# Kernel optimization log

Measured on AMD Instinct MI355X. Metric: run time of the kernel, lower is better.

The kernel has to match this reference:

```python
import jax, jax.numpy as jnp
import numpy as np

NH = 8  # num_heads
EPS_LN = 1e-5
BN_DENOM = float(np.sqrt(1.0 + 1e-5))  # eval-mode BN with running_mean=0, running_var=1


def _layernorm(x, g, b):
    m = jnp.mean(x, axis=-1, keepdims=True)
    v = jnp.var(x, axis=-1, keepdims=True)
    return (x - m) * jax.lax.rsqrt(v + EPS_LN) * g + b


def _rope(q, k):
    # q,k: [B, H, T, D]
    t, d = q.shape[2], q.shape[3]
    half = d // 2
    pos = jnp.arange(t, dtype=q.dtype)[:, None]
    idx = jnp.arange(half, dtype=q.dtype)[None, :]
    inv_freq = 1.0 / (10000.0 ** (idx / half))
    ang = pos * inv_freq  # [T, half]
    sin = jnp.sin(ang)[None, None]
    cos = jnp.cos(ang)[None, None]

    def rot(x):
        x1, x2 = x[..., :half], x[..., half:]
        return jnp.concatenate([x1 * cos - x2 * sin, x1 * sin + x2 * cos], axis=-1)

    return rot(q), rot(k)


def _sep_conv(y, dw, pw):
    # y: [B, C, T]; dw: [C, 1, K]; pw: [O, C]
    c = y.shape[1]
    k = dw.shape[-1]
    y = jax.lax.conv_general_dilated(
        y, dw, window_strides=(2,), padding=[(k // 2, k // 2)],
        dimension_numbers=('NCH', 'OIH', 'NCH'), feature_group_count=c)
    return jnp.einsum('bct,oc->bot', y, pw)


def _attn(h, Wq, bq, Wk, bk, Wv, bv, Wo, bo):
    b, t, e = h.shape
    hd = e // NH
    scale = hd ** -0.5

    def split(z):
        return jnp.transpose(z.reshape(b, t, NH, hd), (0, 2, 1, 3))

    q = split(h @ Wq.T + bq)
    k = split(h @ Wk.T + bk)
    v = split(h @ Wv.T + bv)
    q, k = _rope(q, k)
    logits = jnp.einsum('bhtd,bhsd->bhts', q, k) * scale
    attn = jax.nn.softmax(logits, axis=-1)
    ctx = jnp.einsum('bhts,bhsd->bhtd', attn, v)
    ctx = jnp.transpose(ctx, (0, 2, 1, 3)).reshape(b, t, e)
    return ctx @ Wo.T + bo


def setup_inputs() -> dict:
    key = jax.random.key(0)
    ks = jax.random.split(key, 40)
    B, T, Cin = 8, 4096, 64
    E, L, MLP = 256, 6, 1024
    s = 0.02
    p = {}
    p['x'] = jax.random.normal(ks[0], (B, T, Cin), jnp.float32)
    p['conv1_dw'] = jax.random.normal(ks[1], (Cin, 1, 7), jnp.float32) * s
    p['conv1_pw'] = jax.random.normal(ks[2], (64, Cin), jnp.float32) * s
    p['bn1_g'] = jnp.ones((64,), jnp.float32)
    p['bn1_b'] = jnp.zeros((64,), jnp.float32)
    p['conv2_dw'] = jax.random.normal(ks[3], (64, 1, 7), jnp.float32) * s
    p['conv2_pw'] = jax.random.normal(ks[4], (128, 64), jnp.float32) * s
    p['bn2_g'] = jnp.ones((128,), jnp.float32)
    p['bn2_b'] = jnp.zeros((128,), jnp.float32)
    p['proj_w'] = jax.random.normal(ks[5], (E, 128), jnp.float32) * s
    p['proj_b'] = jnp.zeros((E,), jnp.float32)
    p['cls_tok'] = jax.random.normal(ks[6], (1, 1, E), jnp.float32) * s
    p['Wq'] = jax.random.normal(ks[7], (L, E, E), jnp.float32) * s
    p['bq'] = jnp.zeros((L, E), jnp.float32)
    p['Wk'] = jax.random.normal(ks[8], (L, E, E), jnp.float32) * s
    p['bk'] = jnp.zeros((L, E), jnp.float32)
    p['Wv'] = jax.random.normal(ks[9], (L, E, E), jnp.float32) * s
    p['bv'] = jnp.zeros((L, E), jnp.float32)
    p['Wo'] = jax.random.normal(ks[10], (L, E, E), jnp.float32) * s
    p['bo'] = jnp.zeros((L, E), jnp.float32)
    p['ln1_g'] = jnp.ones((L, E), jnp.float32)
    p['ln1_b'] = jnp.zeros((L, E), jnp.float32)
    p['mlp_w1'] = jax.random.normal(ks[11], (L, MLP, E), jnp.float32) * s
    p['mlp_b1'] = jnp.zeros((L, MLP), jnp.float32)
    p['mlp_w2'] = jax.random.normal(ks[12], (L, E, MLP), jnp.float32) * s
    p['mlp_b2'] = jnp.zeros((L, E), jnp.float32)
    p['ln2_g'] = jnp.ones((L, E), jnp.float32)
    p['ln2_b'] = jnp.zeros((L, E), jnp.float32)
    p['lat_w'] = jax.random.normal(ks[13], (E, E), jnp.float32) * s
    p['lat_b'] = jnp.zeros((E,), jnp.float32)
    p['latn_g'] = jnp.ones((E,), jnp.float32)
    p['latn_b'] = jnp.zeros((E,), jnp.float32)
    p['ts_w'] = jax.random.normal(ks[14], (1, E), jnp.float32) * s
    p['ts_b'] = jnp.zeros((1,), jnp.float32)
    return p


def reference(x, conv1_dw, conv1_pw, bn1_g, bn1_b, conv2_dw, conv2_pw, bn2_g, bn2_b,
              proj_w, proj_b, cls_tok, Wq, bq, Wk, bk, Wv, bv, Wo, bo,
              ln1_g, ln1_b, mlp_w1, mlp_b1, mlp_w2, mlp_b2, ln2_g, ln2_b,
              lat_w, lat_b, latn_g, latn_b, ts_w, ts_b):
    B = x.shape[0]
    y = jnp.transpose(x, (0, 2, 1))  # [B, C, T]
    y = _sep_conv(y, conv1_dw, conv1_pw)
    y = (y / BN_DENOM) * bn1_g[None, :, None] + bn1_b[None, :, None]
    y = jax.nn.gelu(y, approximate=False)
    y = _sep_conv(y, conv2_dw, conv2_pw)
    y = (y / BN_DENOM) * bn2_g[None, :, None] + bn2_b[None, :, None]
    y = jax.nn.gelu(y, approximate=False)
    y = jnp.transpose(y, (0, 2, 1))  # [B, T', 128]
    h = y @ proj_w.T + proj_b  # [B, T', E]
    h = jnp.concatenate([jnp.broadcast_to(cls_tok, (B, 1, h.shape[-1])), h], axis=1)
    L = Wq.shape[0]
    for i in range(L):
        a = _attn(h, Wq[i], bq[i], Wk[i], bk[i], Wv[i], bv[i], Wo[i], bo[i])
        h = _layernorm(h + a, ln1_g[i], ln1_b[i])
        m = jax.nn.gelu(h @ mlp_w1[i].T + mlp_b1[i], approximate=False) @ mlp_w2[i].T + mlp_b2[i]
        h = _layernorm(h + m, ln2_g[i], ln2_b[i])
    h = _layernorm(h @ lat_w.T + lat_b, latn_g, latn_b)
    logits = h[:, 1:] @ ts_w.T + ts_b  # per-time-step logits (CLS excluded)
    return logits
```

## Files before the change

### kernel.cpp

```cpp
#include <hip/hip_runtime.h>
#include <hip/hip_bf16.h>
#include <math.h>

typedef __hip_bfloat16 bf16;
typedef __attribute__((ext_vector_type(8))) short bf16x8_t;
typedef __attribute__((ext_vector_type(4))) short bf16x4_t;
typedef __attribute__((ext_vector_type(4))) float f32x4_t;

#define BN_RDENOM 0.9999950000374997f
#define EPS_LN 1e-5f
#define ATTN_SCALE 0.17677669529663687f
#define S_LEN 1025
#define S_PAD 1088
#define E_DIM 256
#define NHEAD 8
#define HDIM 32
#define MROWS (8 * S_LEN)

__device__ __forceinline__ float bf(const bf16 v) { return __bfloat162float(v); }
__device__ __forceinline__ bf16 tobf(float v) { return __float2bfloat16(v); }
__device__ __forceinline__ short bfbits(float v) {
    bf16 t = __float2bfloat16(v); short s; __builtin_memcpy(&s, &t, 2); return s;
}
__device__ __forceinline__ float gelu_exact(float x) {
    return 0.5f * x * (1.0f + erff(x * 0.70710678118654752f));
}

#define DPP_ROR(x, N) __int_as_float(__builtin_amdgcn_update_dpp(0, __float_as_int(x), 0x120 + (N), 0xF, 0xF, false))
__device__ __forceinline__ float row_allsum(float x) {
    x = x + DPP_ROR(x, 1);
    x = x + DPP_ROR(x, 2);
    x = x + DPP_ROR(x, 4);
    x = x + DPP_ROR(x, 8);
    return x;
}

__global__ __launch_bounds__(256) void cvt_w(const float* __restrict__ src,
    bf16* __restrict__ dst, int n)
{
    int i = (blockIdx.x * 256 + threadIdx.x) * 4;
    if (i >= n) return;
    f32x4_t v = *(const f32x4_t*)(src + i);
    bf16x4_t o;
    #pragma unroll
    for (int j = 0; j < 4; ++j) o[j] = bfbits(v[j]);
    *(bf16x4_t*)((short*)dst + i) = o;
}

__global__ __launch_bounds__(256) void cvt_layer(const float* __restrict__ wq,
    const float* __restrict__ wk, const float* __restrict__ wv, const float* __restrict__ wo,
    const float* __restrict__ w1, const float* __restrict__ w2, bf16* __restrict__ dst)
{
    int i = (blockIdx.x * 256 + threadIdx.x) * 4;
    const float* s; int off;
    if (i < 262144) {
        s = (i < 65536) ? wq : (i < 131072) ? wk : (i < 196608) ? wv : wo;
        off = i & 65535;
    } else if (i < 524288) { s = w1; off = i - 262144; }
    else                   { s = w2; off = i - 524288; }
    f32x4_t v = *(const f32x4_t*)(s + off);
    bf16x4_t o;
    #pragma unroll
    for (int j = 0; j < 4; ++j) o[j] = bfbits(v[j]);
    *(bf16x4_t*)((short*)dst + i) = o;
}

__global__ __launch_bounds__(256) void conv_sep1(const float* __restrict__ x,
    const float* __restrict__ dw, const float* __restrict__ pw,
    const float* __restrict__ g, const float* __restrict__ bb,
    bf16* __restrict__ out)
{
    __shared__ float xs[70][64];
    __shared__ float dy[32][64];
    __shared__ float pws[64][65];
    __shared__ float dws[64][7];
    int blk = blockIdx.x;
    int tile = blk & 63, b = blk >> 6;
    int t0 = tile * 32;
    int tid = threadIdx.x;
    int tbase = t0 * 2 - 3;
    for (int i = tid; i < 70 * 64; i += 256) {
        int r = i >> 6, c = i & 63;
        int t = tbase + r;
        xs[r][c] = (t >= 0 && t < 4096) ? x[((size_t)b * 4096 + t) * 64 + c] : 0.f;
    }
    for (int i = tid; i < 64 * 7; i += 256) dws[i / 7][i % 7] = dw[i];
    for (int i = tid; i < 64 * 64; i += 256) pws[i >> 6][i & 63] = pw[i];
    __syncthreads();
    for (int i = tid; i < 32 * 64; i += 256) {
        int tl = i >> 6, c = i & 63;
        float s = 0.f;
        #pragma unroll
        for (int j = 0; j < 7; ++j) s += xs[2 * tl + j][c] * dws[c][j];
        dy[tl][c] = s;
    }
    __syncthreads();
    for (int i = tid; i < 32 * 64; i += 256) {
        int tl = i >> 6, o = i & 63;
        float s = 0.f;
        #pragma unroll 8
        for (int c = 0; c < 64; ++c) s += dy[tl][c] * pws[o][c];
        s = s * BN_RDENOM * g[o] + bb[o];
        out[((size_t)(b * 2048 + t0 + tl)) * 64 + o] = tobf(gelu_exact(s));
    }
}

__global__ __launch_bounds__(256) void conv_sep2(const bf16* __restrict__ x,
    const float* __restrict__ dw, const float* __restrict__ pw,
    const float* __restrict__ g, const float* __restrict__ bb,
    bf16* __restrict__ out)
{
    __shared__ float xs[70][64];
    __shared__ float dy[32][64];
    __shared__ float pws[128][65];
    __shared__ float dws[64][7];
    int blk = blockIdx.x;
    int tile = blk & 31, b = blk >> 5;
    int t0 = tile * 32;
    int tid = threadIdx.x;
    int tbase = t0 * 2 - 3;
    for (int i = tid; i < 70 * 64; i += 256) {
        int r = i >> 6, c = i & 63;
        int t = tbase + r;
        xs[r][c] = (t >= 0 && t < 2048) ? bf(x[((size_t)b * 2048 + t) * 64 + c]) : 0.f;
    }
    for (int i = tid; i < 64 * 7; i += 256) dws[i / 7][i % 7] = dw[i];
    for (int i = tid; i < 128 * 64; i += 256) pws[i >> 6][i & 63] = pw[i];
    __syncthreads();
    for (int i = tid; i < 32 * 64; i += 256) {
        int tl = i >> 6, c = i & 63;
        float s = 0.f;
        #pragma unroll
        for (int j = 0; j < 7; ++j) s += xs[2 * tl + j][c] * dws[c][j];
        dy[tl][c] = s;
    }
    __syncthreads();
    for (int i = tid; i < 32 * 128; i += 256) {
        int tl = i >> 7, o = i & 127;
        float s = 0.f;
        #pragma unroll 8
        for (int c = 0; c < 64; ++c) s += dy[tl][c] * pws[o][c];
        s = s * BN_RDENOM * g[o] + bb[o];
        out[((size_t)(b * 1024 + t0 + tl)) * 128 + o] = tobf(gelu_exact(s));
    }
}

template <int ACT>
__global__ __launch_bounds__(256) void gemm_bf(const bf16* __restrict__ A,
    const bf16* __restrict__ W, const float* __restrict__ bias,
    bf16* __restrict__ C, int M, int N, int K)
{
    __shared__ short As[64 * 72];
    __shared__ short Bs[64 * 72];
    int tid = threadIdx.x;
    int wave = tid >> 6, lane = tid & 63, quad = lane >> 4, l16 = lane & 15;
    int wm = wave & 1, wn = wave >> 1;
    int m0 = blockIdx.x * 64, n0 = blockIdx.y * 64;

    f32x4_t zero4 = {0.f, 0.f, 0.f, 0.f};
    f32x4_t acc[2][2];
    acc[0][0] = zero4; acc[0][1] = zero4; acc[1][0] = zero4; acc[1][1] = zero4;

    int srow = tid >> 2, skc = (tid & 3) * 16;
    for (int k0 = 0; k0 < K; k0 += 64) {
        {
            int m = m0 + srow;
            bf16x8_t a0 = {}, a1 = {};
            if (m < M) {
                a0 = *(const bf16x8_t*)(A + (size_t)m * K + k0 + skc);
                a1 = *(const bf16x8_t*)(A + (size_t)m * K + k0 + skc + 8);
            }
            *(bf16x8_t*)(&As[srow * 72 + skc])     = a0;
            *(bf16x8_t*)(&As[srow * 72 + skc + 8]) = a1;
        }
        {
            const bf16* wp = W + (size_t)(n0 + srow) * K + k0 + skc;
            *(bf16x8_t*)(&Bs[srow * 72 + skc])     = *(const bf16x8_t*)(wp);
            *(bf16x8_t*)(&Bs[srow * 72 + skc + 8]) = *(const bf16x8_t*)(wp + 8);
        }
        __syncthreads();
        #pragma unroll
        for (int ks = 0; ks < 2; ++ks) {
            bf16x8_t a[2], b[2];
            #pragma unroll
            for (int mi = 0; mi < 2; ++mi)
                a[mi] = *(bf16x8_t*)(&As[(wm * 32 + mi * 16 + l16) * 72 + ks * 32 + quad * 8]);
            #pragma unroll
            for (int ni = 0; ni < 2; ++ni)
                b[ni] = *(bf16x8_t*)(&Bs[(wn * 32 + ni * 16 + l16) * 72 + ks * 32 + quad * 8]);
            #pragma unroll
            for (int mi = 0; mi < 2; ++mi)
                #pragma unroll
                for (int ni = 0; ni < 2; ++ni)
                    acc[mi][ni] = __builtin_amdgcn_mfma_f32_16x16x32_bf16(a[mi], b[ni], acc[mi][ni], 0, 0, 0);
        }
        __syncthreads();
    }
    #pragma unroll
    for (int mi = 0; mi < 2; ++mi) {
        #pragma unroll
        for (int ni = 0; ni < 2; ++ni) {
            int col = n0 + wn * 32 + ni * 16 + l16;
            float bv = bias[col];
            #pragma unroll
            for (int r = 0; r < 4; ++r) {
                int row = m0 + wm * 32 + mi * 16 + quad * 4 + r;
                if (row < M) {
                    float v = acc[mi][ni][r] + bv;
                    if (ACT == 1) v = gelu_exact(v);
                    C[(size_t)row * N + col] = tobf(v);
                }
            }
        }
    }
}

template <int ACT>
__global__ __launch_bounds__(256) void gemm_bf128(const bf16* __restrict__ A,
    const bf16* __restrict__ W, const float* __restrict__ bias,
    bf16* __restrict__ C, int M, int N, int K)
{
    __shared__ short As[128 * 72];
    __shared__ short Bs[64 * 72];
    int tid = threadIdx.x;
    int wave = tid >> 6, lane = tid & 63, quad = lane >> 4, l16 = lane & 15;
    int wm = wave & 1, wn = wave >> 1;
    int m0 = blockIdx.x * 128, n0 = blockIdx.y * 64;

    f32x4_t zero4 = {0.f, 0.f, 0.f, 0.f};
    f32x4_t acc[4][2];
    #pragma unroll
    for (int i = 0; i < 4; ++i) { acc[i][0] = zero4; acc[i][1] = zero4; }

    int srow = tid >> 2, skc = (tid & 3) * 16;
    for (int k0 = 0; k0 < K; k0 += 64) {
        #pragma unroll
        for (int p = 0; p < 2; ++p) {
            int row = srow + p * 64;
            int m = m0 + row;
            bf16x8_t a0 = {}, a1 = {};
            if (m < M) {
                a0 = *(const bf16x8_t*)(A + (size_t)m * K + k0 + skc);
                a1 = *(const bf16x8_t*)(A + (size_t)m * K + k0 + skc + 8);
            }
            *(bf16x8_t*)(&As[row * 72 + skc])     = a0;
            *(bf16x8_t*)(&As[row * 72 + skc + 8]) = a1;
        }
        {
            const bf16* wp = W + (size_t)(n0 + srow) * K + k0 + skc;
            *(bf16x8_t*)(&Bs[srow * 72 + skc])     = *(const bf16x8_t*)(wp);
            *(bf16x8_t*)(&Bs[srow * 72 + skc + 8]) = *(const bf16x8_t*)(wp + 8);
        }
        __syncthreads();
        #pragma unroll
        for (int ks = 0; ks < 2; ++ks) {
            bf16x8_t a[4], b[2];
            #pragma unroll
            for (int mi = 0; mi < 4; ++mi)
                a[mi] = *(bf16x8_t*)(&As[(wm * 64 + mi * 16 + l16) * 72 + ks * 32 + quad * 8]);
            #pragma unroll
            for (int ni = 0; ni < 2; ++ni)
                b[ni] = *(bf16x8_t*)(&Bs[(wn * 32 + ni * 16 + l16) * 72 + ks * 32 + quad * 8]);
            #pragma unroll
            for (int mi = 0; mi < 4; ++mi)
                #pragma unroll
                for (int ni = 0; ni < 2; ++ni)
                    acc[mi][ni] = __builtin_amdgcn_mfma_f32_16x16x32_bf16(a[mi], b[ni], acc[mi][ni], 0, 0, 0);
        }
        __syncthreads();
    }
    #pragma unroll
    for (int mi = 0; mi < 4; ++mi) {
        #pragma unroll
        for (int ni = 0; ni < 2; ++ni) {
            int col = n0 + wn * 32 + ni * 16 + l16;
            float bv = bias[col];
            #pragma unroll
            for (int r = 0; r < 4; ++r) {
                int row = m0 + wm * 64 + mi * 16 + quad * 4 + r;
                if (row < M) {
                    float v = acc[mi][ni][r] + bv;
                    if (ACT == 1) v = gelu_exact(v);
                    C[(size_t)row * N + col] = tobf(v);
                }
            }
        }
    }
}

__global__ __launch_bounds__(256) void gemm_qkv(const bf16* __restrict__ A,
    const bf16* __restrict__ Wqkv, const float* __restrict__ bq,
    const float* __restrict__ bk, const float* __restrict__ bv,
    bf16* __restrict__ qo, bf16* __restrict__ ko, bf16* __restrict__ vo, int M)
{
    const int K = 256, N = 256;
    __shared__ short As[64 * 72];
    __shared__ short Bs[64 * 72];
    int part = blockIdx.y >> 2;
    int n0 = (blockIdx.y & 3) * 64;
    const bf16* W     = Wqkv + (size_t)part * 65536;
    const float* bias = (part == 0) ? bq : (part == 1) ? bk : bv;
    bf16* C           = (part == 0) ? qo : (part == 1) ? ko : vo;
    bool dorope = (part < 2);
    float oscale = (part == 0) ? ATTN_SCALE : 1.0f;

    int tid = threadIdx.x;
    int wave = tid >> 6, lane = tid & 63, quad = lane >> 4, l16 = lane & 15;
    int wm = wave & 1, wn = wave >> 1;
    int m0 = blockIdx.x * 64;

    f32x4_t zero4 = {0.f, 0.f, 0.f, 0.f};
    f32x4_t acc[2][2];
    acc[0][0] = zero4; acc[0][1] = zero4; acc[1][0] = zero4; acc[1][1] = zero4;

    int srow = tid >> 2, skc = (tid & 3) * 16;
    for (int k0 = 0; k0 < K; k0 += 64) {
        {
            int m = m0 + srow;
            bf16x8_t a0 = {}, a1 = {};
            if (m < M) {
                a0 = *(const bf16x8_t*)(A + (size_t)m * K + k0 + skc);
                a1 = *(const bf16x8_t*)(A + (size_t)m * K + k0 + skc + 8);
            }
            *(bf16x8_t*)(&As[srow * 72 + skc])     = a0;
            *(bf16x8_t*)(&As[srow * 72 + skc + 8]) = a1;
        }
        {
            const bf16* wp = W + (size_t)(n0 + srow) * K + k0 + skc;
            *(bf16x8_t*)(&Bs[srow * 72 + skc])     = *(const bf16x8_t*)(wp);
            *(bf16x8_t*)(&Bs[srow * 72 + skc + 8]) = *(const bf16x8_t*)(wp + 8);
        }
        __syncthreads();
        #pragma unroll
        for (int ks = 0; ks < 2; ++ks) {
            bf16x8_t a[2], b[2];
            #pragma unroll
            for (int mi = 0; mi < 2; ++mi)
                a[mi] = *(bf16x8_t*)(&As[(wm * 32 + mi * 16 + l16) * 72 + ks * 32 + quad * 8]);
            #pragma unroll
            for (int ni = 0; ni < 2; ++ni)
                b[ni] = *(bf16x8_t*)(&Bs[(wn * 32 + ni * 16 + l16) * 72 + ks * 32 + quad * 8]);
            #pragma unroll
            for (int mi = 0; mi < 2; ++mi)
                #pragma unroll
                for (int ni = 0; ni < 2; ++ni)
                    acc[mi][ni] = __builtin_amdgcn_mfma_f32_16x16x32_bf16(a[mi], b[ni], acc[mi][ni], 0, 0, 0);
        }
        __syncthreads();
    }
    int col0 = n0 + wn * 32 + l16;
    float b1v = bias[col0], b2v = bias[col0 + 16];
    float invf = powf(10000.f, -(float)l16 * (1.f / 16.f));
    #pragma unroll
    for (int mi = 0; mi < 2; ++mi) {
        #pragma unroll
        for (int r = 0; r < 4; ++r) {
            int row = m0 + wm * 32 + mi * 16 + quad * 4 + r;
            if (row >= M) continue;
            int bb = row / S_LEN, t = row - bb * S_LEN;
            float x1 = acc[mi][0][r] + b1v;
            float x2 = acc[mi][1][r] + b2v;
            if (dorope) {
                float ang = (float)t * invf;
                float sn, cs;
                __sincosf(ang, &sn, &cs);
                float y1 = (x1 * cs - x2 * sn) * oscale;
                float y2 = (x1 * sn + x2 * cs) * oscale;
                x1 = y1; x2 = y2;
            }
            size_t obase = ((size_t)bb * S_PAD + t) * N;
            C[obase + col0]      = tobf(x1);
            C[obase + col0 + 16] = tobf(x2);
        }
    }
}

__global__ __launch_bounds__(256) void assemble_h(const bf16* __restrict__ tmp,
    const float* __restrict__ cls, bf16* __restrict__ h)
{
    int row = blockIdx.x;
    int tid = threadIdx.x;
    int b = row / S_LEN, t = row % S_LEN;
    bf16 v = (t == 0) ? tobf(cls[tid]) : tmp[((size_t)(b * 1024 + t - 1)) * E_DIM + tid];
    h[(size_t)row * E_DIM + tid] = v;
}

__global__ __launch_bounds__(256) void attn_mfma(const bf16* __restrict__ Q,
    const bf16* __restrict__ K, const bf16* __restrict__ V, bf16* __restrict__ O)
{
    __shared__ short VTs[2][32 * 72];
    __shared__ short Ps[4][16 * 72];
    const int NQT = 17;
    int blk = blockIdx.x;
    int qt = blk % NQT;
    int bh = blk / NQT;
    int hh = bh & 7, b = bh >> 3;
    int tid = threadIdx.x;
    int wave = tid >> 6, lane = tid & 63, quad = lane >> 4, l16 = lane & 15;
    int q0 = qt * 64 + wave * 16;
    const size_t bSp = (size_t)b * S_PAD;
    const size_t bS  = (size_t)b * S_LEN;
    const size_t hoff = (size_t)hh * HDIM;
    const bf16* Qb = Q + bSp * E_DIM + hoff;
    const bf16* Kb = K + bSp * E_DIM + hoff;
    const bf16* Vb = V + bSp * E_DIM + hoff;

    f32x4_t zero4 = {0.f, 0.f, 0.f, 0.f};
    bf16x8_t qfrag = *(const bf16x8_t*)(Qb + (size_t)(q0 + l16) * E_DIM + quad * 8);
    f32x4_t o0 = zero4, o1 = zero4;
    float lrun[4] = {0.f, 0.f, 0.f, 0.f};

    int vs = tid >> 2, vd = (tid & 3) * 8;
    short* myP = Ps[wave];

    bf16x8_t vpre = *(const bf16x8_t*)(Vb + (size_t)vs * E_DIM + vd);

    for (int c = 0; c < 17; ++c) {
        int s0 = c * 64;
        short* VT = VTs[c & 1];
        #pragma unroll
        for (int j = 0; j < 8; ++j) VT[(vd + j) * 72 + vs] = vpre[j];
        if (c < 16)
            vpre = *(const bf16x8_t*)(Vb + (size_t)(s0 + 64 + vs) * E_DIM + vd);
        f32x4_t sc[4];
        #pragma unroll
        for (int kk = 0; kk < 4; ++kk) {
            bf16x8_t kf = *(const bf16x8_t*)(Kb + (size_t)(s0 + kk * 16 + l16) * E_DIM + quad * 8);
            sc[kk] = __builtin_amdgcn_mfma_f32_16x16x32_bf16(qfrag, kf, zero4, 0, 0, 0);
        }
        #pragma unroll
        for (int r = 0; r < 4; ++r) {
            float ps = 0.f;
            #pragma unroll
            for (int kk = 0; kk < 4; ++kk) {
                int s = s0 + kk * 16 + l16;
                float raw = (s < S_LEN) ? sc[kk][r] : -1e30f;
                float p = __expf(raw);
                ps += p;
                myP[(quad * 4 + r) * 72 + kk * 16 + l16] = bfbits(p);
            }
            lrun[r] += row_allsum(ps);
        }
        __syncthreads();
        #pragma unroll
        for (int half = 0; half < 2; ++half) {
            int off = half * 32 + quad * 8;
            bf16x8_t pf  = *(bf16x8_t*)(&myP[l16 * 72 + off]);
            bf16x8_t vf0 = *(bf16x8_t*)(&VTs[c & 1][l16 * 72 + off]);
            bf16x8_t vf1 = *(bf16x8_t*)(&VTs[c & 1][(16 + l16) * 72 + off]);
            o0 = __builtin_amdgcn_mfma_f32_16x16x32_bf16(pf, vf0, o0, 0, 0, 0);
            o1 = __builtin_amdgcn_mfma_f32_16x16x32_bf16(pf, vf1, o1, 0, 0, 0);
        }
    }
    #pragma unroll
    for (int r = 0; r < 4; ++r) {
        int qrow = q0 + quad * 4 + r;
        if (qrow < S_LEN) {
            float rs = 1.f / lrun[r];
            O[(bS + qrow) * E_DIM + hoff + l16]      = tobf(o0[r] * rs);
            O[(bS + qrow) * E_DIM + hoff + 16 + l16] = tobf(o1[r] * rs);
        }
    }
}

__global__ __launch_bounds__(256) void ln_kernel(const bf16* __restrict__ X,
    const bf16* __restrict__ R, const float* __restrict__ g,
    const float* __restrict__ b, bf16* __restrict__ out)
{
    int row = blockIdx.x * 4 + (threadIdx.x >> 6);
    int lane = threadIdx.x & 63;
    size_t base = (size_t)row * E_DIM + lane * 4;
    bf16x4_t xv = *(const bf16x4_t*)(X + base);
    float v[4];
    #pragma unroll
    for (int i = 0; i < 4; ++i) { bf16 t; short s = xv[i]; __builtin_memcpy(&t, &s, 2); v[i] = bf(t); }
    if (R) {
        bf16x4_t rv = *(const bf16x4_t*)(R + base);
        #pragma unroll
        for (int i = 0; i < 4; ++i) { bf16 t; short s = rv[i]; __builtin_memcpy(&t, &s, 2); v[i] += bf(t); }
    }
    float s = v[0] + v[1] + v[2] + v[3];
    #pragma unroll
    for (int off = 32; off; off >>= 1) s += __shfl_xor(s, off);
    float mean = s * (1.f / 256.f);
    float var = 0.f;
    #pragma unroll
    for (int i = 0; i < 4; ++i) { v[i] -= mean; var += v[i] * v[i]; }
    #pragma unroll
    for (int off = 32; off; off >>= 1) var += __shfl_xor(var, off);
    float rstd = rsqrtf(var * (1.f / 256.f) + EPS_LN);
    int c = lane * 4;
    bf16x4_t ov;
    #pragma unroll
    for (int i = 0; i < 4; ++i) ov[i] = bfbits(v[i] * rstd * g[c + i] + b[c + i]);
    *(bf16x4_t*)(out + base) = ov;
}

__global__ __launch_bounds__(256) void ts_kernel(const bf16* __restrict__ H,
    const float* __restrict__ w, const float* __restrict__ tb,
    float* __restrict__ out)
{
    int wid = (blockIdx.x << 2) + (threadIdx.x >> 6);
    int lane = threadIdx.x & 63;
    int b = wid >> 10, t = wid & 1023;
    const bf16* row = H + ((size_t)(b * S_LEN + t + 1)) * E_DIM;
    float acc = 0.f;
    for (int e = lane; e < E_DIM; e += 64) acc += bf(row[e]) * w[e];
    #pragma unroll
    for (int off = 32; off; off >>= 1) acc += __shfl_down(acc, off, 64);
    if (lane == 0) out[wid] = acc + tb[0];
}

extern "C" void kernel_launch(void* const* d_in, const int* in_sizes, int n_in,
                              void* d_out, int out_size, void* d_ws, size_t ws_size,
                              hipStream_t stream)
{
    (void)in_sizes; (void)n_in; (void)out_size; (void)ws_size;
    const float* X        = (const float*)d_in[0];
    const float* CONV1_DW = (const float*)d_in[1];
    const float* CONV1_PW = (const float*)d_in[2];
    const float* BN1_G    = (const float*)d_in[3];
    const float* BN1_B    = (const float*)d_in[4];
    const float* CONV2_DW = (const float*)d_in[5];
    const float* CONV2_PW = (const float*)d_in[6];
    const float* BN2_G    = (const float*)d_in[7];
    const float* BN2_B    = (const float*)d_in[8];
    const float* PROJ_W   = (const float*)d_in[9];
    const float* PROJ_B   = (const float*)d_in[10];
    const float* CLS      = (const float*)d_in[11];
    const float* WQ       = (const float*)d_in[12];
    const float* BQ       = (const float*)d_in[13];
    const float* WK       = (const float*)d_in[14];
    const float* BK       = (const float*)d_in[15];
    const float* WV       = (const float*)d_in[16];
    const float* BV       = (const float*)d_in[17];
    const float* WO       = (const float*)d_in[18];
    const float* BO       = (const float*)d_in[19];
    const float* LN1G     = (const float*)d_in[20];
    const float* LN1B     = (const float*)d_in[21];
    const float* W1       = (const float*)d_in[22];
    const float* B1       = (const float*)d_in[23];
    const float* W2       = (const float*)d_in[24];
    const float* B2       = (const float*)d_in[25];
    const float* LN2G     = (const float*)d_in[26];
    const float* LN2B     = (const float*)d_in[27];
    const float* LATW     = (const float*)d_in[28];
    const float* LATB     = (const float*)d_in[29];
    const float* LATNG    = (const float*)d_in[30];
    const float* LATNB    = (const float*)d_in[31];
    const float* TSW      = (const float*)d_in[32];
    const float* TSB      = (const float*)d_in[33];

    const size_t SROW  = (size_t)MROWS * E_DIM;
    const size_t SPROW = (size_t)8 * S_PAD * E_DIM;
    bf16* h    = (bf16*)d_ws;
    bf16* bufB = h + SROW;
    bf16* r0   = bufB + SROW;
    bf16* q  = r0;
    bf16* k  = r0 + SPROW;
    bf16* v  = r0 + 2 * SPROW;
    bf16* cx = r0 + 3 * SPROW;
    bf16* wslot = cx + SROW;
    bf16* y1 = r0;
    bf16* y2 = r0 + SROW;
    bf16* mid = r0;

    conv_sep1<<<dim3(512), dim3(256), 0, stream>>>(X, CONV1_DW, CONV1_PW, BN1_G, BN1_B, y1);
    conv_sep2<<<dim3(256), dim3(256), 0, stream>>>(y1, CONV2_DW, CONV2_PW, BN2_G, BN2_B, y2);
    cvt_w<<<dim3(32), dim3(256), 0, stream>>>(PROJ_W, wslot, 32768);
    gemm_bf<0><<<dim3(128, 4), dim3(256), 0, stream>>>(y2, wslot, PROJ_B, bufB, 8192, 256, 128);
    assemble_h<<<dim3(MROWS), dim3(256), 0, stream>>>(bufB, CLS, h);

    for (int l = 0; l < 6; ++l) {
        cvt_layer<<<dim3(768), dim3(256), 0, stream>>>(
            WQ + (size_t)l * 65536, WK + (size_t)l * 65536, WV + (size_t)l * 65536,
            WO + (size_t)l * 65536, W1 + (size_t)l * 262144, W2 + (size_t)l * 262144, wslot);
        gemm_qkv<<<dim3(129, 12), dim3(256), 0, stream>>>(h, wslot,
            BQ + l * 256, BK + l * 256, BV + l * 256, q, k, v, MROWS);
        attn_mfma<<<dim3(64 * 17), dim3(256), 0, stream>>>(q, k, v, cx);
        gemm_bf<0><<<dim3(129, 4), dim3(256), 0, stream>>>(cx, wslot + 196608, BO + l * 256, bufB, MROWS, 256, 256);
        ln_kernel<<<dim3(MROWS / 4), dim3(256), 0, stream>>>(h, bufB, LN1G + l * 256, LN1B + l * 256, h);
        gemm_bf128<1><<<dim3(65, 16), dim3(256), 0, stream>>>(h, wslot + 262144, B1 + l * 1024, mid, MROWS, 1024, 256);
        gemm_bf<0><<<dim3(129, 4), dim3(256), 0, stream>>>(mid, wslot + 524288, B2 + l * 256, bufB, MROWS, 256, 1024);
        ln_kernel<<<dim3(MROWS / 4), dim3(256), 0, stream>>>(h, bufB, LN2G + l * 256, LN2B + l * 256, h);
    }

    cvt_w<<<dim3(64), dim3(256), 0, stream>>>(LATW, wslot, 65536);
    gemm_bf<0><<<dim3(129, 4), dim3(256), 0, stream>>>(h, wslot, LATB, bufB, MROWS, 256, 256);
    ln_kernel<<<dim3(MROWS / 4), dim3(256), 0, stream>>>(bufB, nullptr, LATNG, LATNB, r0);
    ts_kernel<<<dim3(2048), dim3(256), 0, stream>>>(r0, TSW, TSB, (float*)d_out);
}
```

Baseline: 879.4 us.

## Double-buffer GEMM shared tiles with register prefetch and defer attention row-sum reduction

The three GEMM kernels now use two shared-memory buffers per operand and prefetch the next K-chunk from global memory into registers while the MFMAs run on the current chunk. This removes one barrier per iteration and hides global load latency. In attention, the per-lane partial softmax sums are accumulated locally and reduced across lanes only once at the end, not on every chunk. The cost is double the shared memory per block, which may lower occupancy.

```diff
diff --git a/kernel.cpp b/kernel.cpp
--- a/kernel.cpp
+++ b/kernel.cpp
@@ -150,8 +150,8 @@
     const bf16* __restrict__ W, const float* __restrict__ bias,
     bf16* __restrict__ C, int M, int N, int K)
 {
-    __shared__ short As[64 * 72];
-    __shared__ short Bs[64 * 72];
+    __shared__ short As[2][64 * 72];
+    __shared__ short Bs[2][64 * 72];
     int tid = threadIdx.x;
     int wave = tid >> 6, lane = tid & 63, quad = lane >> 4, l16 = lane & 15;
     int wm = wave & 1, wn = wave >> 1;
@@ -162,39 +162,43 @@
     acc[0][0] = zero4; acc[0][1] = zero4; acc[1][0] = zero4; acc[1][1] = zero4;
 
     int srow = tid >> 2, skc = (tid & 3) * 16;
-    for (int k0 = 0; k0 < K; k0 += 64) {
-        {
-            int m = m0 + srow;
-            bf16x8_t a0 = {}, a1 = {};
-            if (m < M) {
-                a0 = *(const bf16x8_t*)(A + (size_t)m * K + k0 + skc);
-                a1 = *(const bf16x8_t*)(A + (size_t)m * K + k0 + skc + 8);
-            }
-            *(bf16x8_t*)(&As[srow * 72 + skc])     = a0;
-            *(bf16x8_t*)(&As[srow * 72 + skc + 8]) = a1;
-        }
-        {
-            const bf16* wp = W + (size_t)(n0 + srow) * K + k0 + skc;
-            *(bf16x8_t*)(&Bs[srow * 72 + skc])     = *(const bf16x8_t*)(wp);
-            *(bf16x8_t*)(&Bs[srow * 72 + skc + 8]) = *(const bf16x8_t*)(wp + 8);
-        }
+    bool aok = (m0 + srow) < M;
+    const bf16* ap = A + (size_t)(m0 + srow) * K + skc;
+    const bf16* wp = W + (size_t)(n0 + srow) * K + skc;
+
+    bf16x8_t a0 = {}, a1 = {}, b0, b1;
+    if (aok) { a0 = *(const bf16x8_t*)(ap); a1 = *(const bf16x8_t*)(ap + 8); }
+    b0 = *(const bf16x8_t*)(wp); b1 = *(const bf16x8_t*)(wp + 8);
+
+    int nch = K >> 6;
+    for (int c = 0; c < nch; ++c) {
+        short* AsB = As[c & 1];
+        short* BsB = Bs[c & 1];
+        *(bf16x8_t*)(&AsB[srow * 72 + skc])     = a0;
+        *(bf16x8_t*)(&AsB[srow * 72 + skc + 8]) = a1;
+        *(bf16x8_t*)(&BsB[srow * 72 + skc])     = b0;
+        *(bf16x8_t*)(&BsB[srow * 72 + skc + 8]) = b1;
         __syncthreads();
+        if (c + 1 < nch) {
+            int k0 = (c + 1) << 6;
+            if (aok) { a0 = *(const bf16x8_t*)(ap + k0); a1 = *(const bf16x8_t*)(ap + k0 + 8); }
+            b0 = *(const bf16x8_t*)(wp + k0); b1 = *(const bf16x8_t*)(wp + k0 + 8);
+        }
         #pragma unroll
         for (int ks = 0; ks < 2; ++ks) {
             bf16x8_t a[2], b[2];
             #pragma unroll
             for (int mi = 0; mi < 2; ++mi)
-                a[mi] = *(bf16x8_t*)(&As[(wm * 32 + mi * 16 + l16) * 72 + ks * 32 + quad * 8]);
+                a[mi] = *(bf16x8_t*)(&AsB[(wm * 32 + mi * 16 + l16) * 72 + ks * 32 + quad * 8]);
             #pragma unroll
             for (int ni = 0; ni < 2; ++ni)
-                b[ni] = *(bf16x8_t*)(&Bs[(wn * 32 + ni * 16 + l16) * 72 + ks * 32 + quad * 8]);
+                b[ni] = *(bf16x8_t*)(&BsB[(wn * 32 + ni * 16 + l16) * 72 + ks * 32 + quad * 8]);
             #pragma unroll
             for (int mi = 0; mi < 2; ++mi)
                 #pragma unroll
                 for (int ni = 0; ni < 2; ++ni)
                     acc[mi][ni] = __builtin_amdgcn_mfma_f32_16x16x32_bf16(a[mi], b[ni], acc[mi][ni], 0, 0, 0);
         }
-        __syncthreads();
     }
     #pragma unroll
     for (int mi = 0; mi < 2; ++mi) {
@@ -220,8 +224,8 @@
     const bf16* __restrict__ W, const float* __restrict__ bias,
     bf16* __restrict__ C, int M, int N, int K)
 {
-    __shared__ short As[128 * 72];
-    __shared__ short Bs[64 * 72];
+    __shared__ short As[2][128 * 72];
+    __shared__ short Bs[2][64 * 72];
     int tid = threadIdx.x;
     int wave = tid >> 6, lane = tid & 63, quad = lane >> 4, l16 = lane & 15;
     int wm = wave & 1, wn = wave >> 1;
@@ -233,41 +237,48 @@
     for (int i = 0; i < 4; ++i) { acc[i][0] = zero4; acc[i][1] = zero4; }
 
     int srow = tid >> 2, skc = (tid & 3) * 16;
-    for (int k0 = 0; k0 < K; k0 += 64) {
-        #pragma unroll
-        for (int p = 0; p < 2; ++p) {
-            int row = srow + p * 64;
-            int m = m0 + row;
-            bf16x8_t a0 = {}, a1 = {};
-            if (m < M) {
-                a0 = *(const bf16x8_t*)(A + (size_t)m * K + k0 + skc);
-                a1 = *(const bf16x8_t*)(A + (size_t)m * K + k0 + skc + 8);
-            }
-            *(bf16x8_t*)(&As[row * 72 + skc])     = a0;
-            *(bf16x8_t*)(&As[row * 72 + skc + 8]) = a1;
-        }
-        {
-            const bf16* wp = W + (size_t)(n0 + srow) * K + k0 + skc;
-            *(bf16x8_t*)(&Bs[srow * 72 + skc])     = *(const bf16x8_t*)(wp);
-            *(bf16x8_t*)(&Bs[srow * 72 + skc + 8]) = *(const bf16x8_t*)(wp + 8);
-        }
+    bool aok0 = (m0 + srow) < M, aok1 = (m0 + 64 + srow) < M;
+    const bf16* ap0 = A + (size_t)(m0 + srow) * K + skc;
+    const bf16* ap1 = A + (size_t)(m0 + 64 + srow) * K + skc;
+    const bf16* wp  = W + (size_t)(n0 + srow) * K + skc;
+
+    bf16x8_t a00 = {}, a01 = {}, a10 = {}, a11 = {}, b0, b1;
+    if (aok0) { a00 = *(const bf16x8_t*)(ap0); a01 = *(const bf16x8_t*)(ap0 + 8); }
+    if (aok1) { a10 = *(const bf16x8_t*)(ap1); a11 = *(const bf16x8_t*)(ap1 + 8); }
+    b0 = *(const bf16x8_t*)(wp); b1 = *(const bf16x8_t*)(wp + 8);
+
+    int nch = K >> 6;
+    for (int c = 0; c < nch; ++c) {
+        short* AsB = As[c & 1];
+        short* BsB = Bs[c & 1];
+        *(bf16x8_t*)(&AsB[srow * 72 + skc])            = a00;
+        *(bf16x8_t*)(&AsB[srow * 72 + skc + 8])        = a01;
+        *(bf16x8_t*)(&AsB[(64 + srow) * 72 + skc])     = a10;
+        *(bf16x8_t*)(&AsB[(64 + srow) * 72 + skc + 8]) = a11;
+        *(bf16x8_t*)(&BsB[srow * 72 + skc])            = b0;
+        *(bf16x8_t*)(&BsB[srow * 72 + skc + 8])        = b1;
         __syncthreads();
+        if (c + 1 < nch) {
+            int k0 = (c + 1) << 6;
+            if (aok0) { a00 = *(const bf16x8_t*)(ap0 + k0); a01 = *(const bf16x8_t*)(ap0 + k0 + 8); }
+            if (aok1) { a10 = *(const bf16x8_t*)(ap1 + k0); a11 = *(const bf16x8_t*)(ap1 + k0 + 8); }
+            b0 = *(const bf16x8_t*)(wp + k0); b1 = *(const bf16x8_t*)(wp + k0 + 8);
+        }
         #pragma unroll
         for (int ks = 0; ks < 2; ++ks) {
             bf16x8_t a[4], b[2];
             #pragma unroll
             for (int mi = 0; mi < 4; ++mi)
-                a[mi] = *(bf16x8_t*)(&As[(wm * 64 + mi * 16 + l16) * 72 + ks * 32 + quad * 8]);
+                a[mi] = *(bf16x8_t*)(&AsB[(wm * 64 + mi * 16 + l16) * 72 + ks * 32 + quad * 8]);
             #pragma unroll
             for (int ni = 0; ni < 2; ++ni)
-                b[ni] = *(bf16x8_t*)(&Bs[(wn * 32 + ni * 16 + l16) * 72 + ks * 32 + quad * 8]);
+                b[ni] = *(bf16x8_t*)(&BsB[(wn * 32 + ni * 16 + l16) * 72 + ks * 32 + quad * 8]);
             #pragma unroll
             for (int mi = 0; mi < 4; ++mi)
                 #pragma unroll
                 for (int ni = 0; ni < 2; ++ni)
                     acc[mi][ni] = __builtin_amdgcn_mfma_f32_16x16x32_bf16(a[mi], b[ni], acc[mi][ni], 0, 0, 0);
         }
-        __syncthreads();
     }
     #pragma unroll
     for (int mi = 0; mi < 4; ++mi) {
@@ -294,8 +305,8 @@
     bf16* __restrict__ qo, bf16* __restrict__ ko, bf16* __restrict__ vo, int M)
 {
     const int K = 256, N = 256;
-    __shared__ short As[64 * 72];
-    __shared__ short Bs[64 * 72];
+    __shared__ short As[2][64 * 72];
+    __shared__ short Bs[2][64 * 72];
     int part = blockIdx.y >> 2;
     int n0 = (blockIdx.y & 3) * 64;
     const bf16* W     = Wqkv + (size_t)part * 65536;
@@ -314,39 +325,42 @@
     acc[0][0] = zero4; acc[0][1] = zero4; acc[1][0] = zero4; acc[1][1] = zero4;
 
     int srow = tid >> 2, skc = (tid & 3) * 16;
-    for (int k0 = 0; k0 < K; k0 += 64) {
-        {
-            int m = m0 + srow;
-            bf16x8_t a0 = {}, a1 = {};
-            if (m < M) {
-                a0 = *(const bf16x8_t*)(A + (size_t)m * K + k0 + skc);
-                a1 = *(const bf16x8_t*)(A + (size_t)m * K + k0 + skc + 8);
-            }
-            *(bf16x8_t*)(&As[srow * 72 + skc])     = a0;
-            *(bf16x8_t*)(&As[srow * 72 + skc + 8]) = a1;
-        }
-        {
-            const bf16* wp = W + (size_t)(n0 + srow) * K + k0 + skc;
-            *(bf16x8_t*)(&Bs[srow * 72 + skc])     = *(const bf16x8_t*)(wp);
-            *(bf16x8_t*)(&Bs[srow * 72 + skc + 8]) = *(const bf16x8_t*)(wp + 8);
-        }
+    bool aok = (m0 + srow) < M;
+    const bf16* ap = A + (size_t)(m0 + srow) * K + skc;
+    const bf16* wp = W + (size_t)(n0 + srow) * K + skc;
+
+    bf16x8_t a0 = {}, a1 = {}, b0, b1;
+    if (aok) { a0 = *(const bf16x8_t*)(ap); a1 = *(const bf16x8_t*)(ap + 8); }
+    b0 = *(const bf16x8_t*)(wp); b1 = *(const bf16x8_t*)(wp + 8);
+
+    for (int c = 0; c < 4; ++c) {
+        short* AsB = As[c & 1];
+        short* BsB = Bs[c & 1];
+        *(bf16x8_t*)(&AsB[srow * 72 + skc])     = a0;
+        *(bf16x8_t*)(&AsB[srow * 72 + skc + 8]) = a1;
+        *(bf16x8_t*)(&BsB[srow * 72 + skc])     = b0;
+        *(bf16x8_t*)(&BsB[srow * 72 + skc + 8]) = b1;
         __syncthreads();
+        if (c < 3) {
+            int k0 = (c + 1) << 6;
+            if (aok) { a0 = *(const bf16x8_t*)(ap + k0); a1 = *(const bf16x8_t*)(ap + k0 + 8); }
+            b0 = *(const bf16x8_t*)(wp + k0); b1 = *(const bf16x8_t*)(wp + k0 + 8);
+        }
         #pragma unroll
         for (int ks = 0; ks < 2; ++ks) {
             bf16x8_t a[2], b[2];
             #pragma unroll
             for (int mi = 0; mi < 2; ++mi)
-                a[mi] = *(bf16x8_t*)(&As[(wm * 32 + mi * 16 + l16) * 72 + ks * 32 + quad * 8]);
+                a[mi] = *(bf16x8_t*)(&AsB[(wm * 32 + mi * 16 + l16) * 72 + ks * 32 + quad * 8]);
             #pragma unroll
             for (int ni = 0; ni < 2; ++ni)
-                b[ni] = *(bf16x8_t*)(&Bs[(wn * 32 + ni * 16 + l16) * 72 + ks * 32 + quad * 8]);
+                b[ni] = *(bf16x8_t*)(&BsB[(wn * 32 + ni * 16 + l16) * 72 + ks * 32 + quad * 8]);
             #pragma unroll
             for (int mi = 0; mi < 2; ++mi)
                 #pragma unroll
                 for (int ni = 0; ni < 2; ++ni)
                     acc[mi][ni] = __builtin_amdgcn_mfma_f32_16x16x32_bf16(a[mi], b[ni], acc[mi][ni], 0, 0, 0);
         }
-        __syncthreads();
     }
     int col0 = n0 + wn * 32 + l16;
     float b1v = bias[col0], b2v = bias[col0 + 16];
@@ -408,7 +422,7 @@
     f32x4_t zero4 = {0.f, 0.f, 0.f, 0.f};
     bf16x8_t qfrag = *(const bf16x8_t*)(Qb + (size_t)(q0 + l16) * E_DIM + quad * 8);
     f32x4_t o0 = zero4, o1 = zero4;
-    float lrun[4] = {0.f, 0.f, 0.f, 0.f};
+    float lsum[4] = {0.f, 0.f, 0.f, 0.f};
 
     int vs = tid >> 2, vd = (tid & 3) * 8;
     short* myP = Ps[wave];
@@ -439,15 +453,15 @@
                 ps += p;
                 myP[(quad * 4 + r) * 72 + kk * 16 + l16] = bfbits(p);
             }
-            lrun[r] += row_allsum(ps);
+            lsum[r] += ps;
         }
         __syncthreads();
         #pragma unroll
         for (int half = 0; half < 2; ++half) {
             int off = half * 32 + quad * 8;
             bf16x8_t pf  = *(bf16x8_t*)(&myP[l16 * 72 + off]);
-            bf16x8_t vf0 = *(bf16x8_t*)(&VTs[c & 1][l16 * 72 + off]);
-            bf16x8_t vf1 = *(bf16x8_t*)(&VTs[c & 1][(16 + l16) * 72 + off]);
+            bf16x8_t vf0 = *(bf16x8_t*)(&VT[l16 * 72 + off]);
+            bf16x8_t vf1 = *(bf16x8_t*)(&VT[(16 + l16) * 72 + off]);
             o0 = __builtin_amdgcn_mfma_f32_16x16x32_bf16(pf, vf0, o0, 0, 0, 0);
             o1 = __builtin_amdgcn_mfma_f32_16x16x32_bf16(pf, vf1, o1, 0, 0, 0);
         }
@@ -456,7 +470,7 @@
     for (int r = 0; r < 4; ++r) {
         int qrow = q0 + quad * 4 + r;
         if (qrow < S_LEN) {
-            float rs = 1.f / lrun[r];
+            float rs = 1.f / row_allsum(lsum[r]);
             O[(bS + qrow) * E_DIM + hoff + l16]      = tobf(o0[r] * rs);
             O[(bS + qrow) * E_DIM + hoff + 16 + l16] = tobf(o1[r] * rs);
         }
```

Result: slower. 907.9 us (+3.2%).
